# Performance work log

Hardware: AMD Instinct MI355X
Metric: run time of the kernel (lower is better)

The kernel has to match this reference:

```python
import jax, jax.numpy as jnp
import numpy as np

B, H, L, P = 16, 256, 4096, 64  # batch, d_input, seq len (= kernel_size), d_state
R_MIN, R_MAX = 0.9, 1.0         # strong_stability, weak_stability (discrete reservoir radii)


def _as_complex(x):
    # torch.view_as_complex equivalent: trailing dim 2 = (real, imag)
    return x[..., 0] + 1j * x[..., 1]


def setup_inputs() -> dict:
    key = jax.random.key(0)
    ks = jax.random.split(key, 6)
    u = jax.random.normal(ks[0], (B, H, L), jnp.float32)
    C = jax.random.normal(ks[1], (H, P, 2), jnp.float32)       # complex (H,P) as view_as_real
    D = jax.random.normal(ks[2], (H, H), jnp.float32)
    B_bar = jax.random.normal(ks[3], (P, H, 2), jnp.float32)   # complex (P,H) as view_as_real
    # DiscreteStateReservoir: eigenvalues with |lambda| in [strong, weak), uniform phase
    radius = jax.random.uniform(ks[4], (P,), jnp.float32, R_MIN, R_MAX)
    theta = jax.random.uniform(ks[5], (P,), jnp.float32, 0.0, 2.0 * np.pi)
    Lambda_bar = jnp.stack([radius * jnp.cos(theta), radius * jnp.sin(theta)], axis=-1)
    powers = jnp.arange(L, dtype=jnp.float32)
    return {"u": u, "C": C, "D": D, "B_bar": B_bar, "Lambda_bar": Lambda_bar, "powers": powers}


def reference(u, C, D, B_bar, Lambda_bar, powers):
    Cc = _as_complex(C)            # (H, P) complex64
    Bc = _as_complex(B_bar)        # (P, H) complex64
    Lc = _as_complex(Lambda_bar)   # (P,)   complex64
    # Vandermonde: (P, L) = Lambda_bar[p] ** powers[l]
    vand = Lc[:, None] ** powers[None, :]
    # einsum('hp,ph->hp') is elementwise C[h,p]*B_bar[p,h]; then contract over p
    kernel = jnp.einsum('hp,pl->hl', Cc * Bc.T, vand)            # (H, L) complex64
    # circular FFT convolution along L
    y = jnp.fft.ifft(jnp.fft.fft(u, axis=-1) * jnp.fft.fft(kernel, axis=-1)[None], axis=-1)
    # einsum('hh,bhl->bhl', D, u) uses only diag(D)
    y = y.real + jnp.diagonal(D)[None, :, None] * u
    return jnp.tanh(y)
```

## Files before the change

kernel.cpp:

```cpp
#include <hip/hip_runtime.h>
#include <cmath>

#define NF 4096
#define PI2F 6.2831853071795864769f

typedef float2 cf;

__device__ __forceinline__ cf cmulf(cf a, cf b){
  return make_float2(fmaf(a.x, b.x, -(a.y*b.y)), fmaf(a.x, b.y, a.y*b.x));
}

__device__ __forceinline__ int phys(int i){ return i ^ (((i >> 4) & 7) << 1); }

template<int INV>
__device__ __forceinline__ void dft16(cf* v){
  const float C1 = 0.9238795325112867f;
  const float S1 = 0.3826834323650898f;
  const float HF = 0.7071067811865476f;
  cf c[16];
#pragma unroll
  for (int q1 = 0; q1 < 4; ++q1){
    cf a = v[q1], b = v[q1+4], d = v[q1+8], e = v[q1+12];
    cf t0 = make_float2(a.x+d.x, a.y+d.y);
    cf t1 = make_float2(a.x-d.x, a.y-d.y);
    cf t2 = make_float2(b.x+e.x, b.y+e.y);
    cf t3 = make_float2(b.x-e.x, b.y-e.y);
    c[q1*4+0] = make_float2(t0.x+t2.x, t0.y+t2.y);
    c[q1*4+2] = make_float2(t0.x-t2.x, t0.y-t2.y);
    if (!INV){
      c[q1*4+1] = make_float2(t1.x+t3.y, t1.y-t3.x);
      c[q1*4+3] = make_float2(t1.x-t3.y, t1.y+t3.x);
    } else {
      c[q1*4+1] = make_float2(t1.x-t3.y, t1.y+t3.x);
      c[q1*4+3] = make_float2(t1.x+t3.y, t1.y-t3.x);
    }
  }
  {
    auto tw = [&](int i, float wr, float wi){
      float wii = INV ? -wi : wi;
      cf z = c[i];
      c[i] = make_float2(fmaf(z.x, wr, -(z.y*wii)), fmaf(z.x, wii, z.y*wr));
    };
    tw(5,  C1, -S1);
    tw(6,  HF, -HF);
    tw(7,  S1, -C1);
    tw(9,  HF, -HF);
    tw(11,-HF, -HF);
    tw(13, S1, -C1);
    tw(14,-HF, -HF);
    tw(15,-C1,  S1);
    cf z = c[10];
    c[10] = INV ? make_float2(-z.y, z.x) : make_float2(z.y, -z.x);
  }
#pragma unroll
  for (int r0 = 0; r0 < 4; ++r0){
    cf a = c[r0], b = c[4+r0], d = c[8+r0], e = c[12+r0];
    cf t0 = make_float2(a.x+d.x, a.y+d.y);
    cf t1 = make_float2(a.x-d.x, a.y-d.y);
    cf t2 = make_float2(b.x+e.x, b.y+e.y);
    cf t3 = make_float2(b.x-e.x, b.y-e.y);
    v[r0+0] = make_float2(t0.x+t2.x, t0.y+t2.y);
    v[r0+8] = make_float2(t0.x-t2.x, t0.y-t2.y);
    if (!INV){
      v[r0+4]  = make_float2(t1.x+t3.y, t1.y-t3.x);
      v[r0+12] = make_float2(t1.x-t3.y, t1.y+t3.x);
    } else {
      v[r0+4]  = make_float2(t1.x-t3.y, t1.y+t3.x);
      v[r0+12] = make_float2(t1.x+t3.y, t1.y-t3.x);
    }
  }
}

__device__ __forceinline__ void twiddle_apply(cf* v, float ang){
  cf T[16];
  float s, c;
  __sincosf(ang, &s, &c);
  T[1] = make_float2(c, s);
#pragma unroll
  for (int r = 2; r < 16; ++r) T[r] = cmulf(T[r >> 1], T[r - (r >> 1)]);
#pragma unroll
  for (int r = 1; r < 16; ++r) v[r] = cmulf(v[r], T[r]);
}

__device__ __forceinline__ float fast_tanh(float x){
  float e = __expf(2.0f*x);
  return 1.0f - __fdividef(2.0f, e + 1.0f);
}

__global__ void k_vand(const float* __restrict__ Lam, cf* __restrict__ vand){
  int gid = blockIdx.x*256 + threadIdx.x;
  int p = gid >> 12;
  int l = gid & 4095;
  float lr = Lam[2*p], li = Lam[2*p+1];
  double r2 = (double)lr*(double)lr + (double)li*(double)li;
  double lg = 0.5 * log2(r2);
  double tt = atan2((double)li, (double)lr) * 0.15915494309189535;
  double dl = (double)l;
  float mag = exp2f((float)(dl * lg));
  double ph = dl * tt;
  ph -= floor(ph);
  float s, c;
  sincospif((float)(2.0*ph), &s, &c);
  vand[gid] = make_float2(mag*c, mag*s);
}

__global__ __launch_bounds__(512,4) void k_kr(
    const float* __restrict__ C, const float* __restrict__ Bb,
    const cf* __restrict__ vand, float* __restrict__ Kr){
  __shared__ cf Wsh[8][64];
  __shared__ cf Vt[16][512];
  const int t = threadIdx.x;
  const int hg = blockIdx.x >> 3;
  const int ls = blockIdx.x & 7;
  const int h0 = hg*8;
  const int l0 = ls*512;
  {
    int hl = t >> 6, p = t & 63;
    int h = h0 + hl;
    cf cc = ((const cf*)C)[h*64 + p];
    cf bb = ((const cf*)Bb)[p*256 + h];
    Wsh[hl][p] = cmulf(cc, bb);
  }
  float acc[8] = {0,0,0,0,0,0,0,0};
  const int hl = t >> 6;
  const int lane = t & 63;
  for (int pc = 0; pc < 4; ++pc){
    __syncthreads();
    const float4* src = (const float4*)vand;
#pragma unroll
    for (int j = 0; j < 8; ++j){
      int li = j*512 + t;
      int rp = li >> 8;
      int colf4 = li & 255;
      ((float4*)Vt)[li] = src[(size_t)(pc*16 + rp)*2048 + (l0 >> 1) + colf4];
    }
    __syncthreads();
#pragma unroll
    for (int p = 0; p < 16; ++p){
      cf w = Wsh[hl][pc*16 + p];
#pragma unroll
      for (int j = 0; j < 8; ++j){
        cf vv = Vt[p][lane + 64*j];
        acc[j] = fmaf(w.x, vv.x, fmaf(-w.y, vv.y, acc[j]));
      }
    }
  }
  float* dst = Kr + (size_t)(h0 + hl)*NF + l0;
#pragma unroll
  for (int j = 0; j < 8; ++j) dst[lane + 64*j] = acc[j];
}

__global__ __launch_bounds__(256,4) void k_fftkr(
    const float* __restrict__ Kr, const float* __restrict__ D, cf* __restrict__ M){
  __shared__ cf X[4096];
  const int t = threadIdx.x;
  const int h0 = blockIdx.x*2, h1 = h0 + 1;
  const float* k0 = Kr + (size_t)h0*NF;
  const float* k1 = Kr + (size_t)h1*NF;
  cf v[16];
#pragma unroll
  for (int q = 0; q < 16; ++q) v[q] = make_float2(k0[t + 256*q], k1[t + 256*q]);
  dft16<0>(v);
  twiddle_apply(v, -(PI2F/4096.0f)*(float)t);
#pragma unroll
  for (int r = 0; r < 16; ++r) X[phys(t + 256*r)] = v[r];
  __syncthreads();
  const int base = ((t >> 4) << 8) + (t & 15);
#pragma unroll
  for (int q = 0; q < 16; ++q) v[q] = X[phys(base + 16*q)];
  dft16<0>(v);
  twiddle_apply(v, -(PI2F/256.0f)*(float)(t & 15));
#pragma unroll
  for (int r = 0; r < 16; ++r) X[phys(base + 16*r)] = v[r];
  __syncthreads();
  {
    const int s3 = t & 7;
    const float4* X4 = (const float4*)X;
#pragma unroll
    for (int j = 0; j < 8; ++j){
      float4 f = X4[8*t + (j ^ s3)];
      v[2*j]   = make_float2(f.x, f.y);
      v[2*j+1] = make_float2(f.z, f.w);
    }
  }
  dft16<0>(v);
  {
    const int s3 = t & 7;
    float4* X4 = (float4*)X;
#pragma unroll
    for (int j = 0; j < 8; ++j)
      X4[8*t + (j ^ s3)] = make_float4(v[2*j].x, v[2*j].y, v[2*j+1].x, v[2*j+1].y);
  }
  __syncthreads();
  const float dd0 = D[h0*256 + h0];
  const float dd1 = D[h1*256 + h1];
  const float invN = 1.0f/4096.0f;
  cf* M0 = M + (size_t)h0*NF;
  cf* M1 = M + (size_t)h1*NF;
#pragma unroll
  for (int q = 0; q < 16; ++q){
    int idx = 16*t + q;
    cf Z = v[q];
    int k    = ((idx & 15) << 8) | (idx & 240) | (idx >> 8);
    int kc   = (4096 - k) & 4095;
    int pidx = ((kc & 15) << 8) | (kc & 240) | (kc >> 8);
    cf Zp = X[phys(pidx)];
    float KH0r = 0.5f*(Z.x + Zp.x);
    float KH0i = 0.5f*(Z.y - Zp.y);
    float KH1r = 0.5f*(Z.y + Zp.y);
    float KH1i = 0.5f*(Zp.x - Z.x);
    M0[idx] = make_float2((KH0r + dd0)*invN, KH0i*invN);
    M1[idx] = make_float2((KH1r + dd1)*invN, KH1i*invN);
  }
}

__global__ __launch_bounds__(256,4) void k_main(
    const float* __restrict__ u, const cf* __restrict__ M, float* __restrict__ out){
  __shared__ cf X[4096];
  const int t  = threadIdx.x;
  const int h  = blockIdx.x >> 3;
  const int pr = blockIdx.x & 7;
  const size_t row0 = ((size_t)pr*256 + h)*(size_t)NF;
  const size_t row1 = row0 + (size_t)8*256*NF;
  const float* u0 = u + row0;
  const float* u1 = u + row1;
  cf v[16];
#pragma unroll
  for (int q = 0; q < 16; ++q) v[q] = make_float2(u0[t + 256*q], u1[t + 256*q]);
  dft16<0>(v);
  twiddle_apply(v, -(PI2F/4096.0f)*(float)t);
#pragma unroll
  for (int r = 0; r < 16; ++r) X[phys(t + 256*r)] = v[r];
  __syncthreads();
  const int base = ((t >> 4) << 8) + (t & 15);
#pragma unroll
  for (int q = 0; q < 16; ++q) v[q] = X[phys(base + 16*q)];
  dft16<0>(v);
  twiddle_apply(v, -(PI2F/256.0f)*(float)(t & 15));
#pragma unroll
  for (int r = 0; r < 16; ++r) X[phys(base + 16*r)] = v[r];
  __syncthreads();
  const int s3 = t & 7;
  {
    const float4* X4 = (const float4*)X;
#pragma unroll
    for (int j = 0; j < 8; ++j){
      float4 f = X4[8*t + (j ^ s3)];
      v[2*j]   = make_float2(f.x, f.y);
      v[2*j+1] = make_float2(f.z, f.w);
    }
  }
  dft16<0>(v);
  {
    const float4* Mr = (const float4*)(M + (size_t)h*NF + 16*t);
#pragma unroll
    for (int j = 0; j < 8; ++j){
      float4 f = Mr[j];
      v[2*j]   = cmulf(v[2*j],   make_float2(f.x, f.y));
      v[2*j+1] = cmulf(v[2*j+1], make_float2(f.z, f.w));
    }
  }
  dft16<1>(v);
  {
    float4* X4 = (float4*)X;
#pragma unroll
    for (int j = 0; j < 8; ++j)
      X4[8*t + (j ^ s3)] = make_float4(v[2*j].x, v[2*j].y, v[2*j+1].x, v[2*j+1].y);
  }
  __syncthreads();
#pragma unroll
  for (int q = 0; q < 16; ++q) v[q] = X[phys(base + 16*q)];
  twiddle_apply(v, (PI2F/256.0f)*(float)(t & 15));
  dft16<1>(v);
#pragma unroll
  for (int r = 0; r < 16; ++r) X[phys(base + 16*r)] = v[r];
  __syncthreads();
#pragma unroll
  for (int q = 0; q < 16; ++q) v[q] = X[phys(t + 256*q)];
  twiddle_apply(v, (PI2F/4096.0f)*(float)t);
  dft16<1>(v);
  float* o0 = out + row0;
  float* o1 = out + row1;
#pragma unroll
  for (int r = 0; r < 16; ++r){
    o0[t + 256*r] = fast_tanh(v[r].x);
    o1[t + 256*r] = fast_tanh(v[r].y);
  }
}

extern "C" void kernel_launch(void* const* d_in, const int* in_sizes, int n_in,
                              void* d_out, int out_size, void* d_ws, size_t ws_size,
                              hipStream_t stream){
  const float* u   = (const float*)d_in[0];
  const float* C   = (const float*)d_in[1];
  const float* D   = (const float*)d_in[2];
  const float* Bb  = (const float*)d_in[3];
  const float* Lam = (const float*)d_in[4];
  float* out = (float*)d_out;
  char* ws = (char*)d_ws;
  cf*    M    = (cf*)ws;
  cf*    vand = (cf*)(ws + (size_t)(8u << 20));
  float* Kr   = (float*)(ws + (size_t)(10u << 20));

  k_vand <<<dim3(1024), dim3(256), 0, stream>>>(Lam, vand);
  k_kr   <<<dim3(256),  dim3(512), 0, stream>>>(C, Bb, vand, Kr);
  k_fftkr<<<dim3(128),  dim3(256), 0, stream>>>(Kr, D, M);
  k_main <<<dim3(2048), dim3(256), 0, stream>>>(u, M, out);
}
```

Before: 75.94 us.

## Switch main FFT to radix-8 with 512 threads and reorder spectrum layout

The main convolution kernel changes from radix-16 (3 passes, 256 threads, 16 values per thread) to radix-8 (4 passes, 512 threads, 8 values per thread). The goal is lower register pressure and higher occupancy. The kernel-spectrum writer now stores M in a digit-reversed order to match the new radix-8 layout. Twiddles are now generated with a Chebyshev recurrence instead of repeated complex products, and shared-memory padding replaces the XOR swizzle. In exchange the kernel makes more shared-memory round trips and barriers, and the recurrence may lose some accuracy.

```diff
diff --git a/kernel.cpp b/kernel.cpp
--- a/kernel.cpp
+++ b/kernel.cpp
@@ -9,8 +9,53 @@
 __device__ __forceinline__ cf cmulf(cf a, cf b){
   return make_float2(fmaf(a.x, b.x, -(a.y*b.y)), fmaf(a.x, b.y, a.y*b.x));
 }
-
-__device__ __forceinline__ int phys(int i){ return i ^ (((i >> 4) & 7) << 1); }
+__device__ __forceinline__ cf cadd(cf a, cf b){ return make_float2(a.x+b.x, a.y+b.y); }
+__device__ __forceinline__ cf csub(cf a, cf b){ return make_float2(a.x-b.x, a.y-b.y); }
+
+__device__ __forceinline__ int phys8(int i){ return i + (i >> 3); }
+__device__ __forceinline__ int phys16(int i){ return i ^ (((i >> 4) & 7) << 1); }
+
+__device__ __forceinline__ int rev8(int i){
+  return ((i & 7) << 9) | (((i >> 3) & 7) << 6) | (((i >> 6) & 7) << 3) | ((i >> 9) & 7);
+}
+
+template<int INV>
+__device__ __forceinline__ void dft8(cf* v){
+  const float HF = 0.7071067811865476f;
+  cf e0,e1,e2,e3,o0,o1,o2,o3;
+  {
+    cf t0 = cadd(v[0], v[4]);
+    cf t1 = csub(v[0], v[4]);
+    cf t2 = cadd(v[2], v[6]);
+    cf t3 = csub(v[2], v[6]);
+    e0 = cadd(t0,t2); e2 = csub(t0,t2);
+    if (!INV){ e1 = make_float2(t1.x+t3.y, t1.y-t3.x); e3 = make_float2(t1.x-t3.y, t1.y+t3.x); }
+    else     { e1 = make_float2(t1.x-t3.y, t1.y+t3.x); e3 = make_float2(t1.x+t3.y, t1.y-t3.x); }
+  }
+  {
+    cf t0 = cadd(v[1], v[5]);
+    cf t1 = csub(v[1], v[5]);
+    cf t2 = cadd(v[3], v[7]);
+    cf t3 = csub(v[3], v[7]);
+    o0 = cadd(t0,t2); o2 = csub(t0,t2);
+    if (!INV){ o1 = make_float2(t1.x+t3.y, t1.y-t3.x); o3 = make_float2(t1.x-t3.y, t1.y+t3.x); }
+    else     { o1 = make_float2(t1.x-t3.y, t1.y+t3.x); o3 = make_float2(t1.x+t3.y, t1.y-t3.x); }
+  }
+  cf w1, w2, w3;
+  if (!INV){
+    w1 = make_float2(HF*(o1.x + o1.y), HF*(o1.y - o1.x));
+    w2 = make_float2(o2.y, -o2.x);
+    w3 = make_float2(HF*(o3.y - o3.x), -HF*(o3.x + o3.y));
+  } else {
+    w1 = make_float2(HF*(o1.x - o1.y), HF*(o1.y + o1.x));
+    w2 = make_float2(-o2.y, o2.x);
+    w3 = make_float2(-HF*(o3.x + o3.y), HF*(o3.x - o3.y));
+  }
+  v[0] = cadd(e0,o0); v[4] = csub(e0,o0);
+  v[1] = cadd(e1,w1); v[5] = csub(e1,w1);
+  v[2] = cadd(e2,w2); v[6] = csub(e2,w2);
+  v[3] = cadd(e3,w3); v[7] = csub(e3,w3);
+}
 
 template<int INV>
 __device__ __forceinline__ void dft16(cf* v){
@@ -71,13 +116,30 @@
   }
 }
 
-__device__ __forceinline__ void twiddle_apply(cf* v, float ang){
-  cf T[16];
+__device__ __forceinline__ void twiddle8(cf* v, float ang){
   float s, c;
   __sincosf(ang, &s, &c);
+  float c2 = 2.0f * c;
+  cf T[8];
   T[1] = make_float2(c, s);
-#pragma unroll
-  for (int r = 2; r < 16; ++r) T[r] = cmulf(T[r >> 1], T[r - (r >> 1)]);
+  T[2] = make_float2(fmaf(c2, c, -1.0f), c2 * s);
+#pragma unroll
+  for (int r = 3; r < 8; ++r)
+    T[r] = make_float2(fmaf(c2, T[r-1].x, -T[r-2].x), fmaf(c2, T[r-1].y, -T[r-2].y));
+#pragma unroll
+  for (int r = 1; r < 8; ++r) v[r] = cmulf(v[r], T[r]);
+}
+
+__device__ __forceinline__ void twiddle16(cf* v, float ang){
+  float s, c;
+  __sincosf(ang, &s, &c);
+  float c2 = 2.0f * c;
+  cf T[16];
+  T[1] = make_float2(c, s);
+  T[2] = make_float2(fmaf(c2, c, -1.0f), c2 * s);
+#pragma unroll
+  for (int r = 3; r < 16; ++r)
+    T[r] = make_float2(fmaf(c2, T[r-1].x, -T[r-2].x), fmaf(c2, T[r-1].y, -T[r-2].y));
 #pragma unroll
   for (int r = 1; r < 16; ++r) v[r] = cmulf(v[r], T[r]);
 }
@@ -155,23 +217,23 @@
   __shared__ cf X[4096];
   const int t = threadIdx.x;
   const int h0 = blockIdx.x*2, h1 = h0 + 1;
-  const float* k0 = Kr + (size_t)h0*NF;
-  const float* k1 = Kr + (size_t)h1*NF;
+  const float* k0p = Kr + (size_t)h0*NF;
+  const float* k1p = Kr + (size_t)h1*NF;
   cf v[16];
 #pragma unroll
-  for (int q = 0; q < 16; ++q) v[q] = make_float2(k0[t + 256*q], k1[t + 256*q]);
+  for (int q = 0; q < 16; ++q) v[q] = make_float2(k0p[t + 256*q], k1p[t + 256*q]);
   dft16<0>(v);
-  twiddle_apply(v, -(PI2F/4096.0f)*(float)t);
-#pragma unroll
-  for (int r = 0; r < 16; ++r) X[phys(t + 256*r)] = v[r];
+  twiddle16(v, -(PI2F/4096.0f)*(float)t);
+#pragma unroll
+  for (int r = 0; r < 16; ++r) X[phys16(t + 256*r)] = v[r];
   __syncthreads();
   const int base = ((t >> 4) << 8) + (t & 15);
 #pragma unroll
-  for (int q = 0; q < 16; ++q) v[q] = X[phys(base + 16*q)];
+  for (int q = 0; q < 16; ++q) v[q] = X[phys16(base + 16*q)];
   dft16<0>(v);
-  twiddle_apply(v, -(PI2F/256.0f)*(float)(t & 15));
-#pragma unroll
-  for (int r = 0; r < 16; ++r) X[phys(base + 16*r)] = v[r];
+  twiddle16(v, -(PI2F/256.0f)*(float)(t & 15));
+#pragma unroll
+  for (int r = 0; r < 16; ++r) X[phys16(base + 16*r)] = v[r];
   __syncthreads();
   {
     const int s3 = t & 7;
@@ -204,19 +266,20 @@
     int k    = ((idx & 15) << 8) | (idx & 240) | (idx >> 8);
     int kc   = (4096 - k) & 4095;
     int pidx = ((kc & 15) << 8) | (kc & 240) | (kc >> 8);
-    cf Zp = X[phys(pidx)];
+    cf Zp = X[phys16(pidx)];
     float KH0r = 0.5f*(Z.x + Zp.x);
     float KH0i = 0.5f*(Z.y - Zp.y);
     float KH1r = 0.5f*(Z.y + Zp.y);
     float KH1i = 0.5f*(Zp.x - Z.x);
-    M0[idx] = make_float2((KH0r + dd0)*invN, KH0i*invN);
-    M1[idx] = make_float2((KH1r + dd1)*invN, KH1i*invN);
-  }
-}
-
-__global__ __launch_bounds__(256,4) void k_main(
+    int w = rev8(k);
+    M0[w] = make_float2((KH0r + dd0)*invN, KH0i*invN);
+    M1[w] = make_float2((KH1r + dd1)*invN, KH1i*invN);
+  }
+}
+
+__global__ __launch_bounds__(512,8) void k_main(
     const float* __restrict__ u, const cf* __restrict__ M, float* __restrict__ out){
-  __shared__ cf X[4096];
+  __shared__ cf X[4608];
   const int t  = threadIdx.x;
   const int h  = blockIdx.x >> 3;
   const int pr = blockIdx.x & 7;
@@ -224,67 +287,78 @@
   const size_t row1 = row0 + (size_t)8*256*NF;
   const float* u0 = u + row0;
   const float* u1 = u + row1;
-  cf v[16];
-#pragma unroll
-  for (int q = 0; q < 16; ++q) v[q] = make_float2(u0[t + 256*q], u1[t + 256*q]);
-  dft16<0>(v);
-  twiddle_apply(v, -(PI2F/4096.0f)*(float)t);
-#pragma unroll
-  for (int r = 0; r < 16; ++r) X[phys(t + 256*r)] = v[r];
-  __syncthreads();
-  const int base = ((t >> 4) << 8) + (t & 15);
-#pragma unroll
-  for (int q = 0; q < 16; ++q) v[q] = X[phys(base + 16*q)];
-  dft16<0>(v);
-  twiddle_apply(v, -(PI2F/256.0f)*(float)(t & 15));
-#pragma unroll
-  for (int r = 0; r < 16; ++r) X[phys(base + 16*r)] = v[r];
-  __syncthreads();
-  const int s3 = t & 7;
-  {
-    const float4* X4 = (const float4*)X;
-#pragma unroll
-    for (int j = 0; j < 8; ++j){
-      float4 f = X4[8*t + (j ^ s3)];
-      v[2*j]   = make_float2(f.x, f.y);
-      v[2*j+1] = make_float2(f.z, f.w);
-    }
-  }
-  dft16<0>(v);
-  {
-    const float4* Mr = (const float4*)(M + (size_t)h*NF + 16*t);
-#pragma unroll
-    for (int j = 0; j < 8; ++j){
-      float4 f = Mr[j];
-      v[2*j]   = cmulf(v[2*j],   make_float2(f.x, f.y));
-      v[2*j+1] = cmulf(v[2*j+1], make_float2(f.z, f.w));
-    }
-  }
-  dft16<1>(v);
-  {
-    float4* X4 = (float4*)X;
-#pragma unroll
-    for (int j = 0; j < 8; ++j)
-      X4[8*t + (j ^ s3)] = make_float4(v[2*j].x, v[2*j].y, v[2*j+1].x, v[2*j+1].y);
-  }
-  __syncthreads();
-#pragma unroll
-  for (int q = 0; q < 16; ++q) v[q] = X[phys(base + 16*q)];
-  twiddle_apply(v, (PI2F/256.0f)*(float)(t & 15));
-  dft16<1>(v);
-#pragma unroll
-  for (int r = 0; r < 16; ++r) X[phys(base + 16*r)] = v[r];
-  __syncthreads();
-#pragma unroll
-  for (int q = 0; q < 16; ++q) v[q] = X[phys(t + 256*q)];
-  twiddle_apply(v, (PI2F/4096.0f)*(float)t);
-  dft16<1>(v);
+  cf v[8];
+#pragma unroll
+  for (int q = 0; q < 8; ++q) v[q] = make_float2(u0[t + 512*q], u1[t + 512*q]);
+  dft8<0>(v);
+  twiddle8(v, -(PI2F/4096.0f)*(float)t);
+#pragma unroll
+  for (int r = 0; r < 8; ++r) X[phys8(t + 512*r)] = v[r];
+  __syncthreads();
+  const int b2 = ((t >> 6) << 9) | (t & 63);
+#pragma unroll
+  for (int q = 0; q < 8; ++q) v[q] = X[phys8(b2 + 64*q)];
+  dft8<0>(v);
+  twiddle8(v, -(PI2F/512.0f)*(float)(t & 63));
+#pragma unroll
+  for (int r = 0; r < 8; ++r) X[phys8(b2 + 64*r)] = v[r];
+  __syncthreads();
+  const int b3 = ((t >> 3) << 6) | (t & 7);
+#pragma unroll
+  for (int q = 0; q < 8; ++q) v[q] = X[phys8(b3 + 8*q)];
+  dft8<0>(v);
+  twiddle8(v, -(PI2F/64.0f)*(float)(t & 7));
+#pragma unroll
+  for (int r = 0; r < 8; ++r) X[phys8(b3 + 8*r)] = v[r];
+  __syncthreads();
+  float4 mf0, mf1;
+  {
+    const float4* Mr = (const float4*)(M + (size_t)h*NF + 8*t);
+    mf0 = Mr[0]; mf1 = Mr[1];
+  }
+#pragma unroll
+  for (int q = 0; q < 8; ++q) v[q] = X[phys8(8*t + q)];
+  dft8<0>(v);
+  {
+    const float4* Mr = (const float4*)(M + (size_t)h*NF + 8*t);
+    float4 f2 = Mr[2], f3 = Mr[3];
+    v[0] = cmulf(v[0], make_float2(mf0.x, mf0.y));
+    v[1] = cmulf(v[1], make_float2(mf0.z, mf0.w));
+    v[2] = cmulf(v[2], make_float2(mf1.x, mf1.y));
+    v[3] = cmulf(v[3], make_float2(mf1.z, mf1.w));
+    v[4] = cmulf(v[4], make_float2(f2.x, f2.y));
+    v[5] = cmulf(v[5], make_float2(f2.z, f2.w));
+    v[6] = cmulf(v[6], make_float2(f3.x, f3.y));
+    v[7] = cmulf(v[7], make_float2(f3.z, f3.w));
+  }
+  dft8<1>(v);
+#pragma unroll
+  for (int q = 0; q < 8; ++q) X[phys8(8*t + q)] = v[q];
+  __syncthreads();
+#pragma unroll
+  for (int r = 0; r < 8; ++r) v[r] = X[phys8(b3 + 8*r)];
+  twiddle8(v, (PI2F/64.0f)*(float)(t & 7));
+  dft8<1>(v);
+#pragma unroll
+  for (int q = 0; q < 8; ++q) X[phys8(b3 + 8*q)] = v[q];
+  __syncthreads();
+#pragma unroll
+  for (int r = 0; r < 8; ++r) v[r] = X[phys8(b2 + 64*r)];
+  twiddle8(v, (PI2F/512.0f)*(float)(t & 63));
+  dft8<1>(v);
+#pragma unroll
+  for (int q = 0; q < 8; ++q) X[phys8(b2 + 64*q)] = v[q];
+  __syncthreads();
+#pragma unroll
+  for (int r = 0; r < 8; ++r) v[r] = X[phys8(t + 512*r)];
+  twiddle8(v, (PI2F/4096.0f)*(float)t);
+  dft8<1>(v);
   float* o0 = out + row0;
   float* o1 = out + row1;
 #pragma unroll
-  for (int r = 0; r < 16; ++r){
-    o0[t + 256*r] = fast_tanh(v[r].x);
-    o1[t + 256*r] = fast_tanh(v[r].y);
+  for (int q = 0; q < 8; ++q){
+    o0[t + 512*q] = fast_tanh(v[q].x);
+    o1[t + 512*q] = fast_tanh(v[q].y);
   }
 }
 
@@ -305,5 +379,5 @@
   k_vand <<<dim3(1024), dim3(256), 0, stream>>>(Lam, vand);
   k_kr   <<<dim3(256),  dim3(512), 0, stream>>>(C, Bb, vand, Kr);
   k_fftkr<<<dim3(128),  dim3(256), 0, stream>>>(Kr, D, M);
-  k_main <<<dim3(2048), dim3(256), 0, stream>>>(u, M, out);
-}
+  k_main <<<dim3(2048), dim3(512), 0, stream>>>(u, M, out);
+}
```

Result: faster. 73.40 us (-3.4%).
